# Kernel tuning notes

Measured on AMD Instinct MI355X. Metric: run time of the kernel, lower is better.

Reference implementation:

```python
import jax, jax.numpy as jnp
import numpy as np


def _gelu_tanh(x):
    # matches F.gelu(x, approximate='tanh')
    c = jnp.asarray(0.7978845608028654, x.dtype)  # sqrt(2/pi)
    return 0.5 * x * (1.0 + jnp.tanh(c * (x + 0.044715 * x * x * x)))


def setup_inputs() -> dict:
    key = jax.random.key(0)
    k1, k2, k3 = jax.random.split(key, 3)
    E, T, H, F = 8, 2048, 1024, 4096
    x = jax.random.normal(k1, (E, T, H), dtype=jnp.float32)
    w1 = jax.random.normal(k2, (E, H, F), dtype=jnp.float32) * (1.0 / np.sqrt(H))
    w2 = jax.random.normal(k3, (E, F, H), dtype=jnp.float32) * (1.0 / np.sqrt(F))
    return {"x": x, "w1": w1, "w2": w2}


def reference(x, w1, w2):
    # [E,T,H] @ [E,H,F] -> [E,T,F]
    h = jnp.einsum('eth,ehf->etf', x, w1)
    h = _gelu_tanh(h)
    # [E,T,F] @ [E,F,H] -> [E,T,H]
    return jnp.einsum('etf,efh->eth', h, w2)
```

## Files before the change

kernel.cpp:

```cpp
#include <hip/hip_runtime.h>
#include <stdint.h>


typedef __bf16  bf16x8  __attribute__((ext_vector_type(8)));
typedef float   floatx4 __attribute__((ext_vector_type(4)));

__device__ __forceinline__ uint16_t f2bf(float f) {
    uint32_t u = __float_as_uint(f);
    u += 0x7FFF + ((u >> 16) & 1);
    return (uint16_t)(u >> 16);
}

__device__ __forceinline__ uint32_t pack2bf(float lo, float hi) {
    return (uint32_t)f2bf(lo) | ((uint32_t)f2bf(hi) << 16);
}

__device__ __forceinline__ float gelu_tanh_f(float x) {
    float u2 = 1.5957691216057308f * (x + 0.044715f * x * x * x);
    return x / (1.0f + __expf(-u2));
}

__device__ __forceinline__ void async16(const void* g, void* l) {
    __builtin_amdgcn_global_load_lds(
        (__attribute__((address_space(1))) void*)(g),
        (__attribute__((address_space(3))) void*)(l),
        16, 0, 0);
}

__global__ void cvt_f32_bf16_x4(const float* __restrict__ in,
                                uint16_t* __restrict__ out, int n4) {
    int i = blockIdx.x * blockDim.x + threadIdx.x;
    if (i >= n4) return;
    float4 v = ((const float4*)in)[i];
    ushort4 o;
    o.x = f2bf(v.x); o.y = f2bf(v.y); o.z = f2bf(v.z); o.w = f2bf(v.w);
    ((ushort4*)out)[i] = o;
}

__global__ void transpose_cvt(const float* __restrict__ in,
                              uint16_t* __restrict__ out, int R, int C) {
    __shared__ uint32_t lds32[64][33];
    const int e = blockIdx.z;
    in  += (size_t)e * R * C;
    out += (size_t)e * C * R;
    const int c0 = blockIdx.x * 64, r0 = blockIdx.y * 64;
    const int t = threadIdx.x;

    const int g = t >> 4;
    const int col4 = (t & 15) * 4;
    const float* p = in + (size_t)(r0 + 4 * g) * C + c0 + col4;
    float4 v0 = ((const float4*)(p))[0];
    float4 v1 = ((const float4*)(p + C))[0];
    float4 v2 = ((const float4*)(p + 2 * (size_t)C))[0];
    float4 v3 = ((const float4*)(p + 3 * (size_t)C))[0];

    lds32[col4 + 0][2 * g]     = pack2bf(v0.x, v1.x);
    lds32[col4 + 1][2 * g]     = pack2bf(v0.y, v1.y);
    lds32[col4 + 2][2 * g]     = pack2bf(v0.z, v1.z);
    lds32[col4 + 3][2 * g]     = pack2bf(v0.w, v1.w);
    lds32[col4 + 0][2 * g + 1] = pack2bf(v2.x, v3.x);
    lds32[col4 + 1][2 * g + 1] = pack2bf(v2.y, v3.y);
    lds32[col4 + 2][2 * g + 1] = pack2bf(v2.z, v3.z);
    lds32[col4 + 3][2 * g + 1] = pack2bf(v2.w, v3.w);
    __syncthreads();

    const int c = t >> 2, ch = t & 3;
    uint32_t v[8];
#pragma unroll
    for (int k = 0; k < 8; ++k) v[k] = lds32[c][ch * 8 + k];
    uint16_t* op = out + (size_t)(c0 + c) * R + r0 + ch * 16;
    *(uint4*)(op)     = make_uint4(v[0], v[1], v[2], v[3]);
    *(uint4*)(op + 8) = make_uint4(v[4], v[5], v[6], v[7]);
}

template <bool GELU>
__global__ void gemm_bt(const uint16_t* __restrict__ A,
                        const uint16_t* __restrict__ Bt,
                        void* __restrict__ Cv, int M, int N, int K) {
    __shared__ __attribute__((aligned(16))) uint16_t lds_a[128 * 64];
    __shared__ __attribute__((aligned(16))) uint16_t lds_b[128 * 64];

    const int e = blockIdx.z;
    A  += (size_t)e * M * K;
    Bt += (size_t)e * N * K;
    const size_t cEbase = (size_t)e * M * N;

    const int tid = threadIdx.x;
    const int rowBase = blockIdx.y * 128;
    const int colBase = blockIdx.x * 128;

    const int lane = tid & 63;
    const int wave = tid >> 6;
    const int wr = wave >> 1, wc = wave & 1;
    const int quad = lane >> 4, l15 = lane & 15;

    const int srow  = tid >> 3;
    const int sxor  = ((tid & 7) ^ (srow & 7)) * 8;
    const uint16_t* gA0 = A  + (size_t)(rowBase + srow) * K + sxor;
    const uint16_t* gB0 = Bt + (size_t)(colBase + srow) * K + sxor;
    uint16_t* lA0 = &lds_a[tid * 8];
    uint16_t* lB0 = &lds_b[tid * 8];
    const size_t rstep = (size_t)32 * K;

    floatx4 acc[4][4] = {};

    const int arow = wr * 64 + l15;
    const int brow = wc * 64 + l15;
    const int axor = l15 & 7;

    for (int k0 = 0; k0 < K; k0 += 64) {
#pragma unroll
        for (int i = 0; i < 4; ++i) {
            async16(gA0 + k0 + i * rstep, lA0 + i * 2048);
            async16(gB0 + k0 + i * rstep, lB0 + i * 2048);
        }
        __syncthreads();

#pragma unroll
        for (int s = 0; s < 2; ++s) {
            const int pcA = ((s * 4 + quad) ^ axor) * 8;
            bf16x8 af[4], bfg[4];
#pragma unroll
            for (int i = 0; i < 4; ++i) {
                af[i]  = *(const bf16x8*)&lds_a[(arow + i * 16) * 64 + pcA];
                bfg[i] = *(const bf16x8*)&lds_b[(brow + i * 16) * 64 + pcA];
            }
#pragma unroll
            for (int mi = 0; mi < 4; ++mi)
#pragma unroll
                for (int ni = 0; ni < 4; ++ni)
                    acc[mi][ni] = __builtin_amdgcn_mfma_f32_16x16x32_bf16(
                        af[mi], bfg[ni], acc[mi][ni], 0, 0, 0);
        }
        __syncthreads();
    }

#pragma unroll
    for (int mi = 0; mi < 4; ++mi) {
#pragma unroll
        for (int r = 0; r < 4; ++r) {
            const int row = rowBase + wr * 64 + mi * 16 + quad * 4 + r;
            const size_t base = cEbase + (size_t)row * N + colBase + wc * 64 + l15;
#pragma unroll
            for (int ni = 0; ni < 4; ++ni) {
                float v = acc[mi][ni][r];
                if constexpr (GELU) {
                    ((uint16_t*)Cv)[base + ni * 16] = f2bf(gelu_tanh_f(v));
                } else {
                    ((float*)Cv)[base + ni * 16] = v;
                }
            }
        }
    }
}

extern "C" void kernel_launch(void* const* d_in, const int* in_sizes, int n_in,
                              void* d_out, int out_size, void* d_ws, size_t ws_size,
                              hipStream_t stream) {
    const float* x  = (const float*)d_in[0];
    const float* w1 = (const float*)d_in[1];
    const float* w2 = (const float*)d_in[2];
    float* out = (float*)d_out;

    const int E = 8, T = 2048, H = 1024, F = 4096;

    uint16_t* xb  = (uint16_t*)d_ws;
    uint16_t* w1t = xb  + (size_t)E * T * H;
    uint16_t* w2t = w1t + (size_t)E * F * H;
    uint16_t* h   = w2t + (size_t)E * H * F;

    {
        int n4 = (E * T * H) / 4;
        cvt_f32_bf16_x4<<<n4 / 256, 256, 0, stream>>>(x, xb, n4);
    }
    transpose_cvt<<<dim3(F / 64, H / 64, E), 256, 0, stream>>>(w1, w1t, H, F);
    transpose_cvt<<<dim3(H / 64, F / 64, E), 256, 0, stream>>>(w2, w2t, F, H);

    gemm_bt<true><<<dim3(F / 128, T / 128, E), 256, 0, stream>>>(xb, w1t, h, T, F, H);
    gemm_bt<false><<<dim3(H / 128, T / 128, E), 256, 0, stream>>>(h, w2t, out, T, H, F);
}
```

Measured before the change: 678.6 us.

## Replace GEMM with 256x256 double-buffered 8-phase pipelined MFMA kernel

Swaps the 128x128 single-buffered GEMM for a 256x256 tile kernel with 8 waves, double-buffered LDS and an 8-phase schedule. The schedule interleaves async global-to-LDS loads with LDS reads and MFMA bursts, and raises wave priority around the MFMAs. It also remaps workgroup ids for locality. The goal is to hide memory latency and raise data reuse per tile, at the cost of much higher register and LDS use and fragile hand-placed waitcnt/barrier ordering.

```diff
diff --git a/kernel.cpp b/kernel.cpp
--- a/kernel.cpp
+++ b/kernel.cpp
@@ -26,6 +26,10 @@
         (__attribute__((address_space(3))) void*)(l),
         16, 0, 0);
 }
+
+#define BARF() do { asm volatile("" ::: "memory");               \
+                    __builtin_amdgcn_s_barrier();                \
+                    asm volatile("" ::: "memory"); } while (0)
 
 __global__ void cvt_f32_bf16_x4(const float* __restrict__ in,
                                 uint16_t* __restrict__ out, int n4) {
@@ -73,85 +77,191 @@
     *(uint4*)(op + 8) = make_uint4(v[4], v[5], v[6], v[7]);
 }
 
+template <int QM>
+__device__ __forceinline__ void rdA(bf16x8 (&af)[4][2], const uint16_t* src,
+                                    int c0, int c1) {
+#pragma unroll
+    for (int m = 0; m < 4; ++m) {
+        af[m][0] = *(const bf16x8*)(src + QM * 8192 + m * 1024 + c0);
+        af[m][1] = *(const bf16x8*)(src + QM * 8192 + m * 1024 + c1);
+    }
+}
+
+template <int QN>
+__device__ __forceinline__ void rdB(bf16x8 (&b)[2][2], const uint16_t* src,
+                                    int c0, int c1) {
+#pragma unroll
+    for (int n = 0; n < 2; ++n) {
+        b[n][0] = *(const bf16x8*)(src + QN * 8192 + n * 1024 + c0);
+        b[n][1] = *(const bf16x8*)(src + QN * 8192 + n * 1024 + c1);
+    }
+}
+
+template <int QM, int QN>
+__device__ __forceinline__ void mm16(floatx4 (&acc)[8][4],
+                                     const bf16x8 (&af)[4][2],
+                                     const bf16x8 (&b)[2][2]) {
+    __builtin_amdgcn_s_setprio(1);
+#pragma unroll
+    for (int m = 0; m < 4; ++m)
+#pragma unroll
+        for (int n = 0; n < 2; ++n) {
+            floatx4 c = acc[QM * 4 + m][QN * 2 + n];
+            c = __builtin_amdgcn_mfma_f32_16x16x32_bf16(af[m][0], b[n][0], c, 0, 0, 0);
+            c = __builtin_amdgcn_mfma_f32_16x16x32_bf16(af[m][1], b[n][1], c, 0, 0, 0);
+            acc[QM * 4 + m][QN * 2 + n] = c;
+        }
+    __builtin_amdgcn_s_setprio(0);
+}
+
 template <bool GELU>
-__global__ void gemm_bt(const uint16_t* __restrict__ A,
-                        const uint16_t* __restrict__ Bt,
-                        void* __restrict__ Cv, int M, int N, int K) {
-    __shared__ __attribute__((aligned(16))) uint16_t lds_a[128 * 64];
-    __shared__ __attribute__((aligned(16))) uint16_t lds_b[128 * 64];
-
-    const int e = blockIdx.z;
+__global__ __launch_bounds__(512, 2)
+void gemm_bt_8ph(const uint16_t* __restrict__ A,
+                 const uint16_t* __restrict__ Bt,
+                 void* __restrict__ Cv, int M, int N, int K) {
+    __shared__ __attribute__((aligned(16))) uint16_t lds_a[2][256 * 64];
+    __shared__ __attribute__((aligned(16))) uint16_t lds_b[2][256 * 64];
+
+    const int nx = gridDim.x, ny = gridDim.y;
+    int flat = blockIdx.x + nx * (blockIdx.y + ny * blockIdx.z);
+    const int nwg = nx * ny * (int)gridDim.z;
+    flat = (flat & 7) * (nwg >> 3) + (flat >> 3);
+    const int bx  = flat % nx;
+    const int tmp = flat / nx;
+    const int by  = tmp % ny;
+    const int e   = tmp / ny;
+
     A  += (size_t)e * M * K;
     Bt += (size_t)e * N * K;
     const size_t cEbase = (size_t)e * M * N;
-
-    const int tid = threadIdx.x;
-    const int rowBase = blockIdx.y * 128;
-    const int colBase = blockIdx.x * 128;
-
-    const int lane = tid & 63;
-    const int wave = tid >> 6;
-    const int wr = wave >> 1, wc = wave & 1;
-    const int quad = lane >> 4, l15 = lane & 15;
-
-    const int srow  = tid >> 3;
-    const int sxor  = ((tid & 7) ^ (srow & 7)) * 8;
-    const uint16_t* gA0 = A  + (size_t)(rowBase + srow) * K + sxor;
-    const uint16_t* gB0 = Bt + (size_t)(colBase + srow) * K + sxor;
-    uint16_t* lA0 = &lds_a[tid * 8];
-    uint16_t* lB0 = &lds_b[tid * 8];
-    const size_t rstep = (size_t)32 * K;
-
-    floatx4 acc[4][4] = {};
-
-    const int arow = wr * 64 + l15;
-    const int brow = wc * 64 + l15;
-    const int axor = l15 & 7;
-
-    for (int k0 = 0; k0 < K; k0 += 64) {
-#pragma unroll
-        for (int i = 0; i < 4; ++i) {
-            async16(gA0 + k0 + i * rstep, lA0 + i * 2048);
-            async16(gB0 + k0 + i * rstep, lB0 + i * 2048);
-        }
-        __syncthreads();
-
-#pragma unroll
-        for (int s = 0; s < 2; ++s) {
-            const int pcA = ((s * 4 + quad) ^ axor) * 8;
-            bf16x8 af[4], bfg[4];
-#pragma unroll
-            for (int i = 0; i < 4; ++i) {
-                af[i]  = *(const bf16x8*)&lds_a[(arow + i * 16) * 64 + pcA];
-                bfg[i] = *(const bf16x8*)&lds_b[(brow + i * 16) * 64 + pcA];
-            }
-#pragma unroll
-            for (int mi = 0; mi < 4; ++mi)
-#pragma unroll
-                for (int ni = 0; ni < 4; ++ni)
-                    acc[mi][ni] = __builtin_amdgcn_mfma_f32_16x16x32_bf16(
-                        af[mi], bfg[ni], acc[mi][ni], 0, 0, 0);
-        }
-        __syncthreads();
-    }
-
-#pragma unroll
-    for (int mi = 0; mi < 4; ++mi) {
+    const int rowBase = by * 256, colBase = bx * 256;
+
+    const int tid  = threadIdx.x;
+    const int lane = tid & 63, wave = tid >> 6;
+    const int wm = wave >> 2, wn = wave & 3;
+    const int quad = lane >> 4, l15 = lane & 15, lx = l15 & 7;
+    const int c0 = (quad ^ lx) * 8;
+    const int c1 = ((4 + quad) ^ lx) * 8;
+
+    const size_t K32  = (size_t)32 * K;
+    const size_t K64  = (size_t)64 * K;
+    const size_t K128 = (size_t)128 * K;
+
+    const int sxor = ((tid & 7) ^ ((tid >> 3) & 7)) * 8;
+    const uint16_t* gA = A  + (size_t)(rowBase + (tid >> 3)) * K + sxor;
+    const uint16_t* gB = Bt + (size_t)(colBase + (tid >> 8) * 64 +
+                                       ((tid >> 3) & 31)) * K + sxor;
+
+    uint16_t* sA0 = lds_a[0] + tid * 8;
+    uint16_t* sA1 = lds_a[1] + tid * 8;
+    uint16_t* sB0 = lds_b[0] + tid * 8;
+    uint16_t* sB1 = lds_b[1] + tid * 8;
+
+    const uint16_t* aRd0 = lds_a[0] + wm * 4096 + l15 * 64;
+    const uint16_t* aRd1 = lds_a[1] + wm * 4096 + l15 * 64;
+    const uint16_t* bRd0 = lds_b[0] + wn * 2048 + l15 * 64;
+    const uint16_t* bRd1 = lds_b[1] + wn * 2048 + l15 * 64;
+
+#define STG_A(dst, qmv, koff) do {                                   \
+        const uint16_t* g_ = gA + (qmv) * K64 + (koff);              \
+        async16(g_,        (dst) + (qmv) * 8192);                    \
+        async16(g_ + K128, (dst) + (qmv) * 8192 + 4096); } while (0)
+#define STG_B(dst, qnv, koff) do {                                   \
+        const uint16_t* g_ = gB + (qnv) * K32 + (koff);              \
+        async16(g_,        (dst) + (qnv) * 8192);                    \
+        async16(g_ + K128, (dst) + (qnv) * 8192 + 4096); } while (0)
+#define WAITL0() asm volatile("s_waitcnt lgkmcnt(0)" ::: "memory")
+#define WAITV6() asm volatile("s_waitcnt vmcnt(6)"  ::: "memory")
+
+    floatx4 acc[8][4] = {};
+    bf16x8 af[4][2], bq0[2][2], bq1[2][2];
+
+    const int KT = K >> 6;
+    const int NI = KT >> 1;
+
+    STG_A(sA0, 0, 0); STG_B(sB0, 0, 0); STG_B(sB0, 1, 0); STG_A(sA0, 1, 0);
+    STG_A(sA1, 0, 64); STG_B(sB1, 0, 64); STG_B(sB1, 1, 64);
+    WAITV6();
+    BARF();
+
+#pragma unroll 1
+    for (int i = 0; i < NI; ++i) {
+        const size_t oB = (size_t)(2 * i + 1) * 64;
+        const int t2 = (2 * i + 2 < KT) ? (2 * i + 2) : 0;
+        const size_t o2 = (size_t)t2 * 64;
+        const size_t o3 = o2 + 64;
+
+        rdA<0>(af, aRd0, c0, c1); rdB<0>(bq0, bRd0, c0, c1);
+        STG_A(sA1, 1, oB);
+        BARF(); WAITL0();
+        mm16<0, 0>(acc, af, bq0);
+        BARF();
+
+        rdB<1>(bq1, bRd0, c0, c1);
+        STG_A(sA0, 0, o2);
+        BARF(); WAITL0();
+        mm16<0, 1>(acc, af, bq1);
+        BARF();
+
+        rdA<1>(af, aRd0, c0, c1);
+        STG_B(sB0, 0, o2);
+        BARF(); WAITL0();
+        mm16<1, 0>(acc, af, bq0);
+        BARF();
+
+        STG_B(sB0, 1, o2);
+        WAITV6();
+        BARF();
+        mm16<1, 1>(acc, af, bq1);
+        BARF();
+
+        rdA<0>(af, aRd1, c0, c1); rdB<0>(bq0, bRd1, c0, c1);
+        STG_A(sA0, 1, o2);
+        BARF(); WAITL0();
+        mm16<0, 0>(acc, af, bq0);
+        BARF();
+
+        rdB<1>(bq1, bRd1, c0, c1);
+        STG_A(sA1, 0, o3);
+        BARF(); WAITL0();
+        mm16<0, 1>(acc, af, bq1);
+        BARF();
+
+        rdA<1>(af, aRd1, c0, c1);
+        STG_B(sB1, 0, o3);
+        BARF(); WAITL0();
+        mm16<1, 0>(acc, af, bq0);
+        BARF();
+
+        STG_B(sB1, 1, o3);
+        WAITV6();
+        BARF();
+        mm16<1, 1>(acc, af, bq1);
+        BARF();
+    }
+    asm volatile("s_waitcnt vmcnt(0)" ::: "memory");
+
+#pragma unroll
+    for (int mf = 0; mf < 8; ++mf) {
 #pragma unroll
         for (int r = 0; r < 4; ++r) {
-            const int row = rowBase + wr * 64 + mi * 16 + quad * 4 + r;
-            const size_t base = cEbase + (size_t)row * N + colBase + wc * 64 + l15;
-#pragma unroll
-            for (int ni = 0; ni < 4; ++ni) {
-                float v = acc[mi][ni][r];
+            const int row = rowBase + wm * 128 + mf * 16 + quad * 4 + r;
+            const size_t base = cEbase + (size_t)row * N + colBase + wn * 64 + l15;
+#pragma unroll
+            for (int nf = 0; nf < 4; ++nf) {
+                float v = acc[mf][nf][r];
                 if constexpr (GELU) {
-                    ((uint16_t*)Cv)[base + ni * 16] = f2bf(gelu_tanh_f(v));
+                    ((uint16_t*)Cv)[base + nf * 16] = f2bf(gelu_tanh_f(v));
                 } else {
-                    ((float*)Cv)[base + ni * 16] = v;
+                    ((float*)Cv)[base + nf * 16] = v;
                 }
             }
         }
     }
+#undef STG_A
+#undef STG_B
+#undef WAITL0
+#undef WAITV6
 }
 
 extern "C" void kernel_launch(void* const* d_in, const int* in_sizes, int n_in,
@@ -176,6 +286,6 @@
     transpose_cvt<<<dim3(F / 64, H / 64, E), 256, 0, stream>>>(w1, w1t, H, F);
     transpose_cvt<<<dim3(H / 64, F / 64, E), 256, 0, stream>>>(w2, w2t, F, H);
 
-    gemm_bt<true><<<dim3(F / 128, T / 128, E), 256, 0, stream>>>(xb, w1t, h, T, F, H);
-    gemm_bt<false><<<dim3(H / 128, T / 128, E), 256, 0, stream>>>(h, w2t, out, T, H, F);
-}
+    gemm_bt_8ph<true ><<<dim3(F / 256, T / 256, E), 512, 0, stream>>>(xb, w1t, h, T, F, H);
+    gemm_bt_8ph<false><<<dim3(H / 256, T / 256, E), 512, 0, stream>>>(h, w2t, out, T, H, F);
+}
```

New measurement: 669.3 us. No clear change (-1.4%).
